# Performance work log

Measured on AMD Instinct MI355X. Metric: run time of the kernel, lower is better.

The kernel has to match this reference:

```python
import jax, jax.numpy as jnp
import numpy as np

N = 100000  # nodes
E = 600000  # edges
D = 128     # input_dim
H = D // 2  # hidden of MLP head
OUT = 10    # output_dim
EPS = 1e-5
NEG_SLOPE = 0.2


def _p(key, shape, scale):
    return jax.random.normal(key, shape, dtype=jnp.float32) * scale


def setup_inputs() -> dict:
    key = jax.random.key(0)
    ks = jax.random.split(key, 16)
    s = 1.0 / np.sqrt(D)
    return {
        "x": jax.random.normal(ks[0], (N, D), dtype=jnp.float32),
        "edge_index": jax.random.randint(ks[1], (2, E), 0, N, dtype=jnp.int64),
        # SAGEConv: lin_l (applied to mean-aggregated neighbors, has bias), lin_r (root)
        "sage_Wl": _p(ks[2], (D, D), s), "sage_Wr": _p(ks[3], (D, D), s),
        "sage_b": jnp.zeros((D,), jnp.float32),
        # GCNConv
        "gcn_W": _p(ks[4], (D, D), s), "gcn_b": jnp.zeros((D,), jnp.float32),
        # GATConv (heads=1)
        "gat_W": _p(ks[5], (D, D), s),
        "gat_att_src": _p(ks[6], (D,), s), "gat_att_dst": _p(ks[7], (D,), s),
        "gat_b": jnp.zeros((D,), jnp.float32),
        # BatchNorms (batch-stat normalization)
        "bn1_g": jnp.ones((D,), jnp.float32), "bn1_b": jnp.zeros((D,), jnp.float32),
        "bn2_g": jnp.ones((D,), jnp.float32), "bn2_b": jnp.zeros((D,), jnp.float32),
        "bn3_g": jnp.ones((D,), jnp.float32), "bn3_b": jnp.zeros((D,), jnp.float32),
        # MLP head
        "lin1_W": _p(ks[8], (D, H), s), "lin1_b": jnp.zeros((H,), jnp.float32),
        "lin2_W": _p(ks[9], (H, OUT), 1.0 / np.sqrt(H)), "lin2_b": jnp.zeros((OUT,), jnp.float32),
    }


def _bn_relu(x, g, b):
    mu = jnp.mean(x, axis=0)
    var = jnp.mean(jnp.square(x - mu), axis=0)
    return jax.nn.relu((x - mu) * jax.lax.rsqrt(var + EPS) * g + b)


def _sage(x, src, dst, Wl, Wr, b):
    agg = jax.ops.segment_sum(x[src], dst, num_segments=N)          # [N, D]
    cnt = jax.ops.segment_sum(jnp.ones((src.shape[0],), x.dtype), dst, num_segments=N)
    mean = agg / jnp.maximum(cnt, 1.0)[:, None]
    return mean @ Wl + x @ Wr + b


def _gcn(x, src, dst, W, b):
    loop = jnp.arange(N, dtype=src.dtype)
    s = jnp.concatenate([src, loop]); d = jnp.concatenate([dst, loop])
    deg = jax.ops.segment_sum(jnp.ones((d.shape[0],), x.dtype), d, num_segments=N)
    dinv = jnp.where(deg > 0, jax.lax.rsqrt(jnp.maximum(deg, 1.0)), 0.0)
    xw = x @ W
    msg = xw[s] * (dinv[s] * dinv[d])[:, None]
    return jax.ops.segment_sum(msg, d, num_segments=N) + b


def _gat(x, src, dst, W, att_s, att_d, b):
    loop = jnp.arange(N, dtype=src.dtype)
    s = jnp.concatenate([src, loop]); d = jnp.concatenate([dst, loop])
    xw = x @ W                                  # [N, D]
    a_s = xw @ att_s                            # [N]
    a_d = xw @ att_d                            # [N]
    e = jax.nn.leaky_relu(a_s[s] + a_d[d], NEG_SLOPE)  # [E+N]
    m = jax.ops.segment_max(e, d, num_segments=N)
    ee = jnp.exp(e - m[d])
    z = jax.ops.segment_sum(ee, d, num_segments=N)
    alpha = ee / z[d]
    return jax.ops.segment_sum(alpha[:, None] * xw[s], d, num_segments=N) + b


def reference(x, edge_index, sage_Wl, sage_Wr, sage_b, gcn_W, gcn_b,
              gat_W, gat_att_src, gat_att_dst, gat_b,
              bn1_g, bn1_b, bn2_g, bn2_b, bn3_g, bn3_b,
              lin1_W, lin1_b, lin2_W, lin2_b):
    src, dst = edge_index[0], edge_index[1]
    h = _bn_relu(_sage(x, src, dst, sage_Wl, sage_Wr, sage_b), bn1_g, bn1_b)
    h = _bn_relu(_gcn(h, src, dst, gcn_W, gcn_b), bn2_g, bn2_b)
    h = _bn_relu(_gat(h, src, dst, gat_W, gat_att_src, gat_att_dst, gat_b), bn3_g, bn3_b)
    # dropout is identity in eval mode
    h = jax.nn.relu(h @ lin1_W + lin1_b) @ lin2_W + lin2_b
    return jax.nn.log_softmax(h, axis=1)
```

## Files before the change

kernel.cpp:

```cpp
#include <hip/hip_runtime.h>

static constexpr int Dd = 128;
static constexpr int Hh = 64;
static constexpr int OC = 10;
#define CDIV(a,b) (((a)+(b)-1)/(b))

typedef __attribute__((ext_vector_type(8))) short short8v;
typedef __attribute__((ext_vector_type(16))) float f32x16;
typedef unsigned short u16;

__device__ __forceinline__ float lrelu(float x){ return x>0.f? x : 0.2f*x; }
__device__ __forceinline__ unsigned f2bf(float f){
  unsigned u = __float_as_uint(f);
  return (u + 0x7FFFu + ((u>>16)&1u)) >> 16;
}
__device__ __forceinline__ float bl(unsigned u){ return __uint_as_float(u<<16); }
__device__ __forceinline__ float bh(unsigned u){ return __uint_as_float(u & 0xFFFF0000u); }

__global__ __launch_bounds__(256) void k_hist(const int* __restrict__ dst, int E,
    int* __restrict__ cnt) {
  int e = blockIdx.x*256 + threadIdx.x;
  if (e < E) atomicAdd(cnt + dst[e], 1);
}

__global__ __launch_bounds__(256) void k_scan_l1(const int* __restrict__ cnt,
    int* __restrict__ rp, int n, int* __restrict__ bsum) {
  __shared__ int sdata[256];
  int t = threadIdx.x;
  int base = blockIdx.x*2048 + t*8;
  int v[8]; int s = 0;
  #pragma unroll
  for (int k = 0; k < 8; k++) { v[k] = (base+k < n) ? cnt[base+k] : 0; s += v[k]; }
  sdata[t] = s; __syncthreads();
  for (int off = 1; off < 256; off <<= 1) {
    int a = sdata[t];
    int b = (t >= off) ? sdata[t-off] : 0;
    __syncthreads();
    sdata[t] = a + b;
    __syncthreads();
  }
  int ex = sdata[t] - s;
  if (t == 255) bsum[blockIdx.x] = sdata[255];
  int run = ex;
  #pragma unroll
  for (int k = 0; k < 8; k++) { if (base+k < n) rp[base+k] = run; run += v[k]; }
}

__global__ void k_scan_l2(int* __restrict__ bsum, int nb) {
  if (threadIdx.x == 0 && blockIdx.x == 0) {
    int run = 0;
    for (int i = 0; i < nb; i++) { int v = bsum[i]; bsum[i] = run; run += v; }
  }
}

__global__ __launch_bounds__(256) void k_scan_l3(int* __restrict__ rp, int n,
    const int* __restrict__ bsum, int E) {
  int off = bsum[blockIdx.x];
  int base = blockIdx.x*2048 + threadIdx.x*8;
  #pragma unroll
  for (int k = 0; k < 8; k++) if (base+k < n) rp[base+k] += off;
  if (blockIdx.x == 0 && threadIdx.x == 0) rp[n] = E;
}

__global__ __launch_bounds__(256) void k_fill(const int* __restrict__ src,
    const int* __restrict__ dst, int E, const int* __restrict__ rp,
    int* __restrict__ cnt, int* __restrict__ col) {
  int e = blockIdx.x*256 + threadIdx.x;
  if (e >= E) return;
  int d = dst[e];
  int pos = rp[d] + atomicSub(cnt + d, 1) - 1;
  col[pos] = src[e];
}

__global__ __launch_bounds__(256) void k_dinv(const int* __restrict__ rp,
    float* __restrict__ dinv, int n) {
  int i = blockIdx.x*256 + threadIdx.x;
  if (i < n) dinv[i] = rsqrtf((float)(rp[i+1] - rp[i]) + 1.0f);
}

__global__ __launch_bounds__(256) void k_wt_all(
    const float* __restrict__ w0, const float* __restrict__ w1,
    const float* __restrict__ w2, const float* __restrict__ w3,
    const float* __restrict__ w4,
    u16* __restrict__ o0, u16* __restrict__ o1, u16* __restrict__ o2,
    u16* __restrict__ o3, u16* __restrict__ o4) {
  int idx = blockIdx.x*256 + threadIdx.x;
  const float* W; u16* O; int base, N;
  if (idx < 65536) {
    int m = idx >> 14;
    W = m==0?w0 : m==1?w1 : m==2?w2 : w3;
    O = m==0?o0 : m==1?o1 : m==2?o2 : o3;
    base = idx & 16383; N = 128;
  } else if (idx < 73728) {
    W = w4; O = o4; base = idx - 65536; N = 64;
  } else return;
  int n = base / 128, k = base % 128;
  int f = (k>>3)*N*8 + n*8 + (k&7);
  O[f] = (u16)f2bf(W[k*N + n]);
}

__global__ __launch_bounds__(256) void k_tobf16(const float* __restrict__ in,
    u16* __restrict__ out, int n8) {
  int idx = blockIdx.x*256 + threadIdx.x;
  if (idx >= n8) return;
  const float4* p = reinterpret_cast<const float4*>(in) + idx*2;
  float4 v0 = p[0], v1 = p[1];
  uint4 w;
  w.x = f2bf(v0.x) | (f2bf(v0.y)<<16);
  w.y = f2bf(v0.z) | (f2bf(v0.w)<<16);
  w.z = f2bf(v1.x) | (f2bf(v1.y)<<16);
  w.w = f2bf(v1.z) | (f2bf(v1.w)<<16);
  reinterpret_cast<uint4*>(out)[idx] = w;
}

__global__ __launch_bounds__(256) void k_sage_gather(const u16* __restrict__ xb,
    const int* __restrict__ rp, const int* __restrict__ col,
    u16* __restrict__ ob, int n) {
  int gid = blockIdx.x*256 + threadIdx.x;
  int i = gid >> 5, l = gid & 31;
  if (i >= n) return;
  int beg = rp[i], end = rp[i+1];
  const u16* xp = xb + l*4;
  float a0=0.f, a1=0.f, a2=0.f, a3=0.f;
  int j = beg;
  for (; j+4 <= end; j += 4) {
    int s0=col[j], s1=col[j+1], s2=col[j+2], s3=col[j+3];
    uint2 v0 = *reinterpret_cast<const uint2*>(xp + (size_t)s0*Dd);
    uint2 v1 = *reinterpret_cast<const uint2*>(xp + (size_t)s1*Dd);
    uint2 v2 = *reinterpret_cast<const uint2*>(xp + (size_t)s2*Dd);
    uint2 v3 = *reinterpret_cast<const uint2*>(xp + (size_t)s3*Dd);
    a0 += (bl(v0.x)+bl(v1.x)) + (bl(v2.x)+bl(v3.x));
    a1 += (bh(v0.x)+bh(v1.x)) + (bh(v2.x)+bh(v3.x));
    a2 += (bl(v0.y)+bl(v1.y)) + (bl(v2.y)+bl(v3.y));
    a3 += (bh(v0.y)+bh(v1.y)) + (bh(v2.y)+bh(v3.y));
  }
  for (; j < end; j++) {
    int s = col[j];
    uint2 v = *reinterpret_cast<const uint2*>(xp + (size_t)s*Dd);
    a0 += bl(v.x); a1 += bh(v.x); a2 += bl(v.y); a3 += bh(v.y);
  }
  float inv = 1.0f / fmaxf((float)(end - beg), 1.0f);
  uint2 o;
  o.x = f2bf(a0*inv) | (f2bf(a1*inv)<<16);
  o.y = f2bf(a2*inv) | (f2bf(a3*inv)<<16);
  *reinterpret_cast<uint2*>(ob + (size_t)i*Dd + l*4) = o;
}

__global__ __launch_bounds__(256) void k_gcn_gather(const u16* __restrict__ xb,
    const int* __restrict__ rp, const int* __restrict__ col,
    const float* __restrict__ dinv, u16* __restrict__ ob, int n) {
  int gid = blockIdx.x*256 + threadIdx.x;
  int i = gid >> 5, l = gid & 31;
  if (i >= n) return;
  int beg = rp[i], end = rp[i+1];
  const u16* xp = xb + l*4;
  float a0=0.f, a1=0.f, a2=0.f, a3=0.f;
  int j = beg;
  for (; j+4 <= end; j += 4) {
    int s0=col[j], s1=col[j+1], s2=col[j+2], s3=col[j+3];
    uint2 v0 = *reinterpret_cast<const uint2*>(xp + (size_t)s0*Dd);
    uint2 v1 = *reinterpret_cast<const uint2*>(xp + (size_t)s1*Dd);
    uint2 v2 = *reinterpret_cast<const uint2*>(xp + (size_t)s2*Dd);
    uint2 v3 = *reinterpret_cast<const uint2*>(xp + (size_t)s3*Dd);
    float w0 = dinv[s0], w1 = dinv[s1], w2 = dinv[s2], w3 = dinv[s3];
    a0 += (w0*bl(v0.x)+w1*bl(v1.x)) + (w2*bl(v2.x)+w3*bl(v3.x));
    a1 += (w0*bh(v0.x)+w1*bh(v1.x)) + (w2*bh(v2.x)+w3*bh(v3.x));
    a2 += (w0*bl(v0.y)+w1*bl(v1.y)) + (w2*bl(v2.y)+w3*bl(v3.y));
    a3 += (w0*bh(v0.y)+w1*bh(v1.y)) + (w2*bh(v2.y)+w3*bh(v3.y));
  }
  for (; j < end; j++) {
    int s = col[j];
    float w = dinv[s];
    uint2 v = *reinterpret_cast<const uint2*>(xp + (size_t)s*Dd);
    a0 += w*bl(v.x); a1 += w*bh(v.x); a2 += w*bl(v.y); a3 += w*bh(v.y);
  }
  float di = dinv[i];
  float ws = di*di;
  uint2 sv = *reinterpret_cast<const uint2*>(xp + (size_t)i*Dd);
  a0 = di*a0 + ws*bl(sv.x); a1 = di*a1 + ws*bh(sv.x);
  a2 = di*a2 + ws*bl(sv.y); a3 = di*a3 + ws*bh(sv.y);
  uint2 o;
  o.x = f2bf(a0) | (f2bf(a1)<<16);
  o.y = f2bf(a2) | (f2bf(a3)<<16);
  *reinterpret_cast<uint2*>(ob + (size_t)i*Dd + l*4) = o;
}

__global__ __launch_bounds__(256) void k_gat_gather(const u16* __restrict__ xb,
    const int* __restrict__ rp, const int* __restrict__ col,
    const float* __restrict__ a_s, const float* __restrict__ a_d,
    u16* __restrict__ ob, int n) {
  int gid = blockIdx.x*256 + threadIdx.x;
  int i = gid >> 5, l = gid & 31;
  if (i >= n) return;
  int beg = rp[i], end = rp[i+1];
  const u16* xp = xb + l*4;
  float ad = a_d[i];
  float m = lrelu(a_s[i] + ad);
  float z = 1.0f;
  uint2 sv = *reinterpret_cast<const uint2*>(xp + (size_t)i*Dd);
  float a0 = bl(sv.x), a1 = bh(sv.x), a2 = bl(sv.y), a3 = bh(sv.y);
  int j = beg;
  for (; j+4 <= end; j += 4) {
    int s0=col[j], s1=col[j+1], s2=col[j+2], s3=col[j+3];
    uint2 v0 = *reinterpret_cast<const uint2*>(xp + (size_t)s0*Dd);
    uint2 v1 = *reinterpret_cast<const uint2*>(xp + (size_t)s1*Dd);
    uint2 v2 = *reinterpret_cast<const uint2*>(xp + (size_t)s2*Dd);
    uint2 v3 = *reinterpret_cast<const uint2*>(xp + (size_t)s3*Dd);
    float e0 = lrelu(a_s[s0]+ad), e1 = lrelu(a_s[s1]+ad);
    float e2 = lrelu(a_s[s2]+ad), e3 = lrelu(a_s[s3]+ad);
    float mg = fmaxf(fmaxf(e0,e1), fmaxf(e2,e3));
    if (mg > m) {
      float r = __expf(m - mg);
      z *= r; a0 *= r; a1 *= r; a2 *= r; a3 *= r;
      m = mg;
    }
    float w0 = __expf(e0-m), w1 = __expf(e1-m);
    float w2 = __expf(e2-m), w3 = __expf(e3-m);
    z += (w0+w1) + (w2+w3);
    a0 += (w0*bl(v0.x)+w1*bl(v1.x)) + (w2*bl(v2.x)+w3*bl(v3.x));
    a1 += (w0*bh(v0.x)+w1*bh(v1.x)) + (w2*bh(v2.x)+w3*bh(v3.x));
    a2 += (w0*bl(v0.y)+w1*bl(v1.y)) + (w2*bl(v2.y)+w3*bl(v3.y));
    a3 += (w0*bh(v0.y)+w1*bh(v1.y)) + (w2*bh(v2.y)+w3*bh(v3.y));
  }
  for (; j < end; j++) {
    int s = col[j];
    uint2 v = *reinterpret_cast<const uint2*>(xp + (size_t)s*Dd);
    float e = lrelu(a_s[s]+ad);
    if (e > m) {
      float r = __expf(m - e);
      z *= r; a0 *= r; a1 *= r; a2 *= r; a3 *= r;
      m = e;
    }
    float w = __expf(e-m);
    z += w;
    a0 += w*bl(v.x); a1 += w*bh(v.x); a2 += w*bl(v.y); a3 += w*bh(v.y);
  }
  float inv = 1.0f / z;
  uint2 o;
  o.x = f2bf(a0*inv) | (f2bf(a1*inv)<<16);
  o.y = f2bf(a2*inv) | (f2bf(a3*inv)<<16);
  *reinterpret_cast<uint2*>(ob + (size_t)i*Dd + l*4) = o;
}

__global__ __launch_bounds__(256) void k_bn_stats_bf(const u16* __restrict__ X, int M,
    float* __restrict__ gsum, float* __restrict__ gsq) {
  __shared__ float ss[2][256];
  int t = threadIdx.x;
  int cd = t & 63;
  int rg = t >> 6;
  float s0=0.f, q0=0.f, s1=0.f, q1=0.f;
  const unsigned* Xu = reinterpret_cast<const unsigned*>(X);
  for (int r = blockIdx.x*4 + rg; r < M; r += gridDim.x*4) {
    unsigned v = Xu[(size_t)r*64 + cd];
    float a = bl(v), b = bh(v);
    s0 += a; q0 += a*a; s1 += b; q1 += b*b;
  }
  ss[0][t] = s0; ss[1][t] = q0; __syncthreads();
  float rs0 = 0.f, rq0 = 0.f;
  if (rg == 0) {
    rs0 = ss[0][cd] + ss[0][cd+64] + ss[0][cd+128] + ss[0][cd+192];
    rq0 = ss[1][cd] + ss[1][cd+64] + ss[1][cd+128] + ss[1][cd+192];
  }
  __syncthreads();
  ss[0][t] = s1; ss[1][t] = q1; __syncthreads();
  if (rg == 0) {
    float rs1 = ss[0][cd] + ss[0][cd+64] + ss[0][cd+128] + ss[0][cd+192];
    float rq1 = ss[1][cd] + ss[1][cd+64] + ss[1][cd+128] + ss[1][cd+192];
    atomicAdd(gsum + 2*cd,     rs0); atomicAdd(gsq + 2*cd,     rq0);
    atomicAdd(gsum + 2*cd + 1, rs1); atomicAdd(gsq + 2*cd + 1, rq1);
  }
}

template<int NCOLS, bool DUAL, bool BNA, bool STATS, bool BIASRELU, bool ATT, bool OUTBF>
__global__ __launch_bounds__(256) void k_mm(
    const u16* __restrict__ A1, const u16* __restrict__ A2,
    const u16* __restrict__ WT1, const u16* __restrict__ WT2,
    const float* __restrict__ bng, const float* __restrict__ bnb,
    const float* __restrict__ bsum_in, const float* __restrict__ bsq_in,
    const float* __restrict__ bias,
    void* __restrict__ Cout, int M,
    float* __restrict__ gsum, float* __restrict__ gsq,
    const float* __restrict__ att_sv, const float* __restrict__ att_dv,
    float* __restrict__ as_out, float* __restrict__ ad_out) {
  constexpr int NF = NCOLS/32;
  __shared__ char ldsW[NCOLS*128*2];
  __shared__ float s_scale[128], s_shift[128];
  int t = threadIdx.x;
  int wave = t >> 6, l = t & 63;
  int lm = l & 31, h = l >> 5;
  int row0 = blockIdx.x*128;

  if constexpr (BNA) {
    if (t < 128) {
      float mu = bsum_in[t] / (float)M;
      float var = fmaxf(bsq_in[t] / (float)M - mu*mu, 0.f);
      float sc = bng[t] * rsqrtf(var + 1e-5f);
      s_scale[t] = sc;
      s_shift[t] = bnb[t] - mu*sc;
    }
  }

  f32x16 acc[NF];
  #pragma unroll
  for (int nf = 0; nf < NF; nf++)
    #pragma unroll
    for (int i = 0; i < 16; i++) acc[nf][i] = 0.f;

  const int arow = row0 + wave*32 + lm;
  const bool rok = arow < M;

  const int nph = DUAL ? 2 : 1;
  for (int ph = 0; ph < nph; ph++) {
    const u16* A = (DUAL && ph) ? A2 : A1;
    const u16* WT = (DUAL && ph) ? WT2 : WT1;
    uint4 araw[8];
    const u16* ap = A + (size_t)arow*128 + h*8;
    #pragma unroll
    for (int ks = 0; ks < 8; ks++) {
      araw[ks] = rok ? *reinterpret_cast<const uint4*>(ap + ks*16)
                     : uint4{0,0,0,0};
    }
    #pragma unroll
    for (int i = 0; i < NCOLS*16/256; i++) {
      int c = i*256 + t;
      reinterpret_cast<uint4*>(ldsW)[c] = reinterpret_cast<const uint4*>(WT)[c];
    }
    __syncthreads();
    short8v af[8];
    #pragma unroll
    for (int ks = 0; ks < 8; ks++) {
      uint4 w = araw[ks];
      if constexpr (BNA) {
        int kbase = ks*16 + h*8;
        float4 sc0 = *reinterpret_cast<const float4*>(&s_scale[kbase]);
        float4 sc1 = *reinterpret_cast<const float4*>(&s_scale[kbase+4]);
        float4 sh0 = *reinterpret_cast<const float4*>(&s_shift[kbase]);
        float4 sh1 = *reinterpret_cast<const float4*>(&s_shift[kbase+4]);
        float e0 = fmaxf(bl(w.x)*sc0.x+sh0.x, 0.f), e1 = fmaxf(bh(w.x)*sc0.y+sh0.y, 0.f);
        float e2 = fmaxf(bl(w.y)*sc0.z+sh0.z, 0.f), e3 = fmaxf(bh(w.y)*sc0.w+sh0.w, 0.f);
        float e4 = fmaxf(bl(w.z)*sc1.x+sh1.x, 0.f), e5 = fmaxf(bh(w.z)*sc1.y+sh1.y, 0.f);
        float e6 = fmaxf(bl(w.w)*sc1.z+sh1.z, 0.f), e7 = fmaxf(bh(w.w)*sc1.w+sh1.w, 0.f);
        w.x = f2bf(e0) | (f2bf(e1)<<16);
        w.y = f2bf(e2) | (f2bf(e3)<<16);
        w.z = f2bf(e4) | (f2bf(e5)<<16);
        w.w = f2bf(e6) | (f2bf(e7)<<16);
      }
      af[ks] = *reinterpret_cast<short8v*>(&w);
    }
    #pragma unroll
    for (int ks = 0; ks < 8; ks++) {
      int kc = ks*2 + h;
      #pragma unroll
      for (int nf = 0; nf < NF; nf++) {
        short8v bf = *reinterpret_cast<short8v*>(ldsW + (kc*NCOLS + nf*32 + lm)*16);
        acc[nf] = __builtin_amdgcn_mfma_f32_32x32x16_bf16(af[ks], bf, acc[nf], 0, 0, 0);
      }
    }
    if (DUAL && ph == 0) __syncthreads();
  }
  float* s_sum = reinterpret_cast<float*>(ldsW);
  float* s_sq  = s_sum + 128;
  if constexpr (STATS) {
    __syncthreads();
    if (t < 128) { s_sum[t] = 0.f; s_sq[t] = 0.f; }
    __syncthreads();
  }
  #pragma unroll
  for (int nf = 0; nf < NF; nf++) {
    int colg = nf*32 + lm;
    float bv = 0.f;
    if constexpr (BIASRELU) bv = bias[colg];
    float ps = 0.f, pq = 0.f;
    #pragma unroll
    for (int reg = 0; reg < 16; reg++) {
      int row = row0 + wave*32 + (reg&3) + 8*(reg>>2) + 4*h;
      float v = acc[nf][reg];
      if constexpr (BIASRELU) v = fmaxf(v + bv, 0.f);
      if (row < M) {
        if constexpr (OUTBF)
          ((u16*)Cout)[(size_t)row*NCOLS + colg] = (u16)f2bf(v);
        else
          ((float*)Cout)[(size_t)row*NCOLS + colg] = v;
      }
      ps += v; pq += v*v;
    }
    if constexpr (STATS) {
      atomicAdd(&s_sum[colg], ps);
      atomicAdd(&s_sq[colg], pq);
    }
  }
  if constexpr (ATT) {
    float as_c[NF], ad_c[NF];
    #pragma unroll
    for (int nf = 0; nf < NF; nf++) { as_c[nf] = att_sv[nf*32+lm]; ad_c[nf] = att_dv[nf*32+lm]; }
    #pragma unroll
    for (int reg = 0; reg < 16; reg++) {
      float ps = 0.f, pd = 0.f;
      #pragma unroll
      for (int nf = 0; nf < NF; nf++) { float v = acc[nf][reg]; ps += v*as_c[nf]; pd += v*ad_c[nf]; }
      #pragma unroll
      for (int mm = 1; mm < 32; mm <<= 1) { ps += __shfl_xor(ps, mm); pd += __shfl_xor(pd, mm); }
      int row = row0 + wave*32 + (reg&3) + 8*(reg>>2) + 4*h;
      if (lm == 0 && row < M) { as_out[row] = ps; ad_out[row] = pd; }
    }
  }
  if constexpr (STATS) {
    __syncthreads();
    if (t < 128) { atomicAdd(gsum + t, s_sum[t]); atomicAdd(gsq + t, s_sq[t]); }
  }
}

__global__ __launch_bounds__(256) void k_head2(const float* __restrict__ M1,
    const float* __restrict__ W2, const float* __restrict__ b2,
    float* __restrict__ out, int n) {
  __shared__ float rows[256][65];
  __shared__ float w2s[Hh][OC];
  __shared__ float b2s[OC];
  int t = threadIdx.x;
  for (int i = t; i < Hh*OC; i += 256) w2s[i/OC][i%OC] = W2[i];
  if (t < OC) b2s[t] = b2[t];
  int r0 = blockIdx.x*256;
  #pragma unroll
  for (int i = 0; i < 16; i++) {
    int f = i*256 + t; int row = f >> 4; int c0 = (f & 15) << 2;
    float4 v = {0,0,0,0};
    if (r0 + row < n) v = *reinterpret_cast<const float4*>(M1 + (size_t)(r0+row)*Hh + c0);
    rows[row][c0+0] = v.x; rows[row][c0+1] = v.y;
    rows[row][c0+2] = v.z; rows[row][c0+3] = v.w;
  }
  __syncthreads();
  int row = r0 + t;
  if (row >= n) return;
  float p[OC];
  #pragma unroll
  for (int c = 0; c < OC; c++) p[c] = b2s[c];
  for (int k = 0; k < Hh; k++) {
    float a = rows[t][k];
    #pragma unroll
    for (int c = 0; c < OC; c++) p[c] += a * w2s[k][c];
  }
  float mx = p[0];
  #pragma unroll
  for (int c = 1; c < OC; c++) mx = fmaxf(mx, p[c]);
  float s = 0.f;
  #pragma unroll
  for (int c = 0; c < OC; c++) s += expf(p[c] - mx);
  float lse = mx + logf(s);
  #pragma unroll
  for (int c = 0; c < OC; c++) out[(size_t)row*OC + c] = p[c] - lse;
}

extern "C" void kernel_launch(void* const* d_in, const int* in_sizes, int n_in,
                              void* d_out, int out_size, void* d_ws, size_t ws_size,
                              hipStream_t stream) {
  const float* x       = (const float*)d_in[0];
  const int*   ei      = (const int*)d_in[1];
  const float* sage_Wl = (const float*)d_in[2];
  const float* sage_Wr = (const float*)d_in[3];
  const float* gcn_W   = (const float*)d_in[5];
  const float* gat_W   = (const float*)d_in[7];
  const float* att_s   = (const float*)d_in[8];
  const float* att_d   = (const float*)d_in[9];
  const float* bn1_g = (const float*)d_in[11], *bn1_b = (const float*)d_in[12];
  const float* bn2_g = (const float*)d_in[13], *bn2_b = (const float*)d_in[14];
  const float* bn3_g = (const float*)d_in[15], *bn3_b = (const float*)d_in[16];
  const float* lin1_W = (const float*)d_in[17], *lin1_b = (const float*)d_in[18];
  const float* lin2_W = (const float*)d_in[19], *lin2_b = (const float*)d_in[20];

  const int Nn = in_sizes[0] / Dd;
  const int Ee = in_sizes[1] / 2;
  const int* srcv = ei;
  const int* dstv = ei + Ee;

  u16* b0 = (u16*)d_ws;
  u16* b1 = b0 + (size_t)Nn*Dd;
  u16* b2 = b1 + (size_t)Nn*Dd;
  float* dinv  = (float*)(b2 + (size_t)Nn*Dd);
  float* a_s   = dinv + Nn;
  float* a_d   = a_s + Nn;
  float* bs    = a_d + Nn;
  float* bs1_sum = bs,        *bs1_sq = bs + 128;
  float* bs2_sum = bs + 256,  *bs2_sq = bs + 384;
  float* bs3_sum = bs + 512,  *bs3_sq = bs + 640;
  int* rp    = (int*)(bs + 768);
  int* cnt_i = rp + (Nn + 1);
  int* bsum  = cnt_i + Nn;
  int* col   = bsum + 64;
  u16* wt_sWl = (u16*)(col + Ee);
  u16* wt_sWr = wt_sWl + 128*128;
  u16* wt_gcn = wt_sWr + 128*128;
  u16* wt_gat = wt_gcn + 128*128;
  u16* wt_l1  = wt_gat + 128*128;

  const dim3 B(256);
  const dim3 Gn(CDIV(Nn, 256));
  const dim3 Gn32(CDIV(Nn*32, 256));
  const dim3 Ge(CDIV(Ee, 256));
  const dim3 Gmm(CDIV(Nn, 128));
  const dim3 Ghead(CDIV(Nn, 256));
  const dim3 Gstat(512);
  const int nscan = CDIV(Nn, 2048);

  hipMemsetAsync(cnt_i, 0, (size_t)Nn*sizeof(int), stream);
  hipMemsetAsync(bs, 0, 768*sizeof(float), stream);

  k_hist<<<Ge, B, 0, stream>>>(dstv, Ee, cnt_i);
  k_scan_l1<<<dim3(nscan), B, 0, stream>>>(cnt_i, rp, Nn, bsum);
  k_scan_l2<<<dim3(1), dim3(64), 0, stream>>>(bsum, nscan);
  k_scan_l3<<<dim3(nscan), B, 0, stream>>>(rp, Nn, bsum, Ee);
  k_fill<<<Ge, B, 0, stream>>>(srcv, dstv, Ee, rp, cnt_i, col);
  k_dinv<<<Gn, B, 0, stream>>>(rp, dinv, Nn);
  k_wt_all<<<dim3(288), B, 0, stream>>>(sage_Wl, sage_Wr, gcn_W, gat_W, lin1_W,
                                        wt_sWl, wt_sWr, wt_gcn, wt_gat, wt_l1);
  k_tobf16<<<dim3(CDIV(Nn*Dd/8, 256)), B, 0, stream>>>(x, b0, Nn*Dd/8);

  k_sage_gather<<<Gn32, B, 0, stream>>>(b0, rp, col, b1, Nn);
  k_mm<128, true, false, true, false, false, true><<<Gmm, B, 0, stream>>>(
      b1, b0, wt_sWl, wt_sWr, nullptr, nullptr, nullptr, nullptr, nullptr,
      b2, Nn, bs1_sum, bs1_sq, nullptr, nullptr, nullptr, nullptr);

  k_mm<128, false, true, false, false, false, true><<<Gmm, B, 0, stream>>>(
      b2, nullptr, wt_gcn, nullptr, bn1_g, bn1_b, bs1_sum, bs1_sq, nullptr,
      b0, Nn, nullptr, nullptr, nullptr, nullptr, nullptr, nullptr);
  k_gcn_gather<<<Gn32, B, 0, stream>>>(b0, rp, col, dinv, b1, Nn);
  k_bn_stats_bf<<<Gstat, B, 0, stream>>>(b1, Nn, bs2_sum, bs2_sq);

  k_mm<128, false, true, false, false, true, true><<<Gmm, B, 0, stream>>>(
      b1, nullptr, wt_gat, nullptr, bn2_g, bn2_b, bs2_sum, bs2_sq, nullptr,
      b2, Nn, nullptr, nullptr, att_s, att_d, a_s, a_d);
  k_gat_gather<<<Gn32, B, 0, stream>>>(b2, rp, col, a_s, a_d, b0, Nn);
  k_bn_stats_bf<<<Gstat, B, 0, stream>>>(b0, Nn, bs3_sum, bs3_sq);

  float* m1 = (float*)b1;
  k_mm<64, false, true, false, true, false, false><<<Gmm, B, 0, stream>>>(
      b0, nullptr, wt_l1, nullptr, bn3_g, bn3_b, bs3_sum, bs3_sq, lin1_b,
      m1, Nn, nullptr, nullptr, nullptr, nullptr, nullptr, nullptr);
  k_head2<<<Ghead, B, 0, stream>>>(m1, lin2_W, lin2_b, (float*)d_out, Nn);
}
```

Measured before the change: 401.8 us.

## Switch matmul to 16x16x32 MFMA with prepacked weights read directly from global

The dense matmul kernel now uses 16x16x32 bf16 MFMA tiles with 64 rows per block instead of 32x32x16 with 128 rows. Weights are pre-packed into the per-lane fragment order so each lane loads its B fragment straight from global or L2, which removes the LDS weight staging and its barrier. Column stats are reduced with shuffles before the shared atomics. This lowers LDS use and register pressure and doubles the block count for better occupancy, at the cost of redundant weight reads from cache in every wave.

```diff
diff --git a/kernel.cpp b/kernel.cpp
--- a/kernel.cpp
+++ b/kernel.cpp
@@ -6,7 +6,7 @@
 #define CDIV(a,b) (((a)+(b)-1)/(b))
 
 typedef __attribute__((ext_vector_type(8))) short short8v;
-typedef __attribute__((ext_vector_type(16))) float f32x16;
+typedef __attribute__((ext_vector_type(4))) float f32x4;
 typedef unsigned short u16;
 
 __device__ __forceinline__ float lrelu(float x){ return x>0.f? x : 0.2f*x; }
@@ -95,8 +95,11 @@
     W = w4; O = o4; base = idx - 65536; N = 64;
   } else return;
   int n = base / 128, k = base % 128;
-  int f = (k>>3)*N*8 + n*8 + (k&7);
-  O[f] = (u16)f2bf(W[k*N + n]);
+  int ks = k >> 5, nf = n >> 4;
+  int lane = (((k >> 3) & 3) << 4) | (n & 15);
+  int NF16 = N >> 4;
+  int fi = (((ks*NF16 + nf)*64 + lane) << 3) | (k & 7);
+  O[fi] = (u16)f2bf(W[k*N + n]);
 }
 
 __global__ __launch_bounds__(256) void k_tobf16(const float* __restrict__ in,
@@ -282,13 +285,13 @@
     float* __restrict__ gsum, float* __restrict__ gsq,
     const float* __restrict__ att_sv, const float* __restrict__ att_dv,
     float* __restrict__ as_out, float* __restrict__ ad_out) {
-  constexpr int NF = NCOLS/32;
-  __shared__ char ldsW[NCOLS*128*2];
+  constexpr int NF = NCOLS/16;
   __shared__ float s_scale[128], s_shift[128];
+  __shared__ float s_sum[128], s_sq[128];
   int t = threadIdx.x;
   int wave = t >> 6, l = t & 63;
-  int lm = l & 31, h = l >> 5;
-  int row0 = blockIdx.x*128;
+  int c16 = l & 15, rg = l >> 4;
+  int row0 = blockIdx.x*64;
 
   if constexpr (BNA) {
     if (t < 128) {
@@ -298,40 +301,37 @@
       s_scale[t] = sc;
       s_shift[t] = bnb[t] - mu*sc;
     }
-  }
-
-  f32x16 acc[NF];
+    __syncthreads();
+  }
+  if constexpr (STATS) {
+    if (t < 128) { s_sum[t] = 0.f; s_sq[t] = 0.f; }
+    __syncthreads();
+  }
+
+  f32x4 acc[NF];
   #pragma unroll
   for (int nf = 0; nf < NF; nf++)
     #pragma unroll
-    for (int i = 0; i < 16; i++) acc[nf][i] = 0.f;
-
-  const int arow = row0 + wave*32 + lm;
+    for (int i = 0; i < 4; i++) acc[nf][i] = 0.f;
+
+  const int arow = row0 + wave*16 + c16;
   const bool rok = arow < M;
 
   const int nph = DUAL ? 2 : 1;
   for (int ph = 0; ph < nph; ph++) {
     const u16* A = (DUAL && ph) ? A2 : A1;
     const u16* WT = (DUAL && ph) ? WT2 : WT1;
-    uint4 araw[8];
-    const u16* ap = A + (size_t)arow*128 + h*8;
-    #pragma unroll
-    for (int ks = 0; ks < 8; ks++) {
-      araw[ks] = rok ? *reinterpret_cast<const uint4*>(ap + ks*16)
-                     : uint4{0,0,0,0};
-    }
-    #pragma unroll
-    for (int i = 0; i < NCOLS*16/256; i++) {
-      int c = i*256 + t;
-      reinterpret_cast<uint4*>(ldsW)[c] = reinterpret_cast<const uint4*>(WT)[c];
-    }
-    __syncthreads();
-    short8v af[8];
-    #pragma unroll
-    for (int ks = 0; ks < 8; ks++) {
+    uint4 araw[4];
+    const u16* ap = A + (size_t)arow*128 + rg*8;
+    #pragma unroll
+    for (int ks = 0; ks < 4; ks++)
+      araw[ks] = rok ? *reinterpret_cast<const uint4*>(ap + ks*32) : uint4{0,0,0,0};
+    short8v af[4];
+    #pragma unroll
+    for (int ks = 0; ks < 4; ks++) {
       uint4 w = araw[ks];
       if constexpr (BNA) {
-        int kbase = ks*16 + h*8;
+        int kbase = ks*32 + rg*8;
         float4 sc0 = *reinterpret_cast<const float4*>(&s_scale[kbase]);
         float4 sc1 = *reinterpret_cast<const float4*>(&s_scale[kbase+4]);
         float4 sh0 = *reinterpret_cast<const float4*>(&s_shift[kbase]);
@@ -347,33 +347,25 @@
       }
       af[ks] = *reinterpret_cast<short8v*>(&w);
     }
-    #pragma unroll
-    for (int ks = 0; ks < 8; ks++) {
-      int kc = ks*2 + h;
+    const short8v* wp = reinterpret_cast<const short8v*>(WT);
+    #pragma unroll
+    for (int ks = 0; ks < 4; ks++) {
       #pragma unroll
       for (int nf = 0; nf < NF; nf++) {
-        short8v bf = *reinterpret_cast<short8v*>(ldsW + (kc*NCOLS + nf*32 + lm)*16);
-        acc[nf] = __builtin_amdgcn_mfma_f32_32x32x16_bf16(af[ks], bf, acc[nf], 0, 0, 0);
+        short8v bf = wp[(ks*NF + nf)*64 + l];
+        acc[nf] = __builtin_amdgcn_mfma_f32_16x16x32_bf16(af[ks], bf, acc[nf], 0, 0, 0);
       }
     }
-    if (DUAL && ph == 0) __syncthreads();
-  }
-  float* s_sum = reinterpret_cast<float*>(ldsW);
-  float* s_sq  = s_sum + 128;
-  if constexpr (STATS) {
-    __syncthreads();
-    if (t < 128) { s_sum[t] = 0.f; s_sq[t] = 0.f; }
-    __syncthreads();
   }
   #pragma unroll
   for (int nf = 0; nf < NF; nf++) {
-    int colg = nf*32 + lm;
+    int colg = nf*16 + c16;
     float bv = 0.f;
     if constexpr (BIASRELU) bv = bias[colg];
     float ps = 0.f, pq = 0.f;
     #pragma unroll
-    for (int reg = 0; reg < 16; reg++) {
-      int row = row0 + wave*32 + (reg&3) + 8*(reg>>2) + 4*h;
+    for (int reg = 0; reg < 4; reg++) {
+      int row = row0 + wave*16 + rg*4 + reg;
       float v = acc[nf][reg];
       if constexpr (BIASRELU) v = fmaxf(v + bv, 0.f);
       if (row < M) {
@@ -385,23 +377,24 @@
       ps += v; pq += v*v;
     }
     if constexpr (STATS) {
-      atomicAdd(&s_sum[colg], ps);
-      atomicAdd(&s_sq[colg], pq);
+      ps += __shfl_xor(ps, 16); ps += __shfl_xor(ps, 32);
+      pq += __shfl_xor(pq, 16); pq += __shfl_xor(pq, 32);
+      if (rg == 0) { atomicAdd(&s_sum[colg], ps); atomicAdd(&s_sq[colg], pq); }
     }
   }
   if constexpr (ATT) {
     float as_c[NF], ad_c[NF];
     #pragma unroll
-    for (int nf = 0; nf < NF; nf++) { as_c[nf] = att_sv[nf*32+lm]; ad_c[nf] = att_dv[nf*32+lm]; }
-    #pragma unroll
-    for (int reg = 0; reg < 16; reg++) {
+    for (int nf = 0; nf < NF; nf++) { as_c[nf] = att_sv[nf*16+c16]; ad_c[nf] = att_dv[nf*16+c16]; }
+    #pragma unroll
+    for (int reg = 0; reg < 4; reg++) {
       float ps = 0.f, pd = 0.f;
       #pragma unroll
       for (int nf = 0; nf < NF; nf++) { float v = acc[nf][reg]; ps += v*as_c[nf]; pd += v*ad_c[nf]; }
       #pragma unroll
-      for (int mm = 1; mm < 32; mm <<= 1) { ps += __shfl_xor(ps, mm); pd += __shfl_xor(pd, mm); }
-      int row = row0 + wave*32 + (reg&3) + 8*(reg>>2) + 4*h;
-      if (lm == 0 && row < M) { as_out[row] = ps; ad_out[row] = pd; }
+      for (int mm = 1; mm < 16; mm <<= 1) { ps += __shfl_xor(ps, mm); pd += __shfl_xor(pd, mm); }
+      int row = row0 + wave*16 + rg*4 + reg;
+      if (c16 == 0 && row < M) { as_out[row] = ps; ad_out[row] = pd; }
     }
   }
   if constexpr (STATS) {
@@ -496,7 +489,7 @@
   const dim3 Gn(CDIV(Nn, 256));
   const dim3 Gn32(CDIV(Nn*32, 256));
   const dim3 Ge(CDIV(Ee, 256));
-  const dim3 Gmm(CDIV(Nn, 128));
+  const dim3 Gmm(CDIV(Nn, 64));
   const dim3 Ghead(CDIV(Nn, 256));
   const dim3 Gstat(512);
   const int nscan = CDIV(Nn, 2048);
```

New measurement: 404.8 us. Within noise of the previous version (+0.7%).
